# Kernel optimization log

Measured on AMD Instinct MI355X. Metric: run time of the kernel, lower is better.

## Reference

```python
import jax, jax.numpy as jnp
import numpy as np

N = 50000       # nodes
E = 800000      # edges
IN_DIM = 256    # input_dim
HEADS = 4
CH = 32         # per-head channels (hidden_dim; conv3 uses latent_dim//heads = 32 too)
HC = HEADS * CH # 128
ED = 32         # edge_dims


def setup_inputs():
    key = jax.random.key(0)
    ks = iter(jax.random.split(key, 64))
    def nrm(shape):
        return jax.random.normal(next(ks), shape, dtype=jnp.float32) * 0.05
    inp = {}
    inp["x"] = nrm((N, IN_DIM))
    inp["edge_index"] = jax.random.randint(next(ks), (2, E), 0, N)
    inp["attr"] = nrm((E, ED))
    for l, ind in ((1, IN_DIM), (2, HC), (3, HC)):
        inp[f"Wq{l}"] = nrm((ind, HC)); inp[f"bq{l}"] = jnp.zeros((HC,), jnp.float32)
        inp[f"Wk{l}"] = nrm((ind, HC)); inp[f"bk{l}"] = jnp.zeros((HC,), jnp.float32)
        inp[f"Wv{l}"] = nrm((ind, HC)); inp[f"bv{l}"] = jnp.zeros((HC,), jnp.float32)
        inp[f"We{l}"] = nrm((ED, HC))  # lin_edge has no bias in PyG TransformerConv
        inp[f"Ws{l}"] = nrm((ind, HC)); inp[f"bs{l}"] = jnp.zeros((HC,), jnp.float32)
    inp["g1"] = jnp.ones((HC,), jnp.float32); inp["be1"] = jnp.zeros((HC,), jnp.float32)
    inp["g2"] = jnp.ones((HC,), jnp.float32); inp["be2"] = jnp.zeros((HC,), jnp.float32)
    return inp


def _transformer_conv(x, src, dst, attr, Wq, bq, Wk, bk, Wv, bv, We, Ws, bs):
    # PyG TransformerConv, concat=True, root_weight=True, beta=False, dropout=0 (eval).
    q = (x @ Wq + bq).reshape(-1, HEADS, CH)   # [N,H,C] (queries at dst)
    k = (x @ Wk + bk).reshape(-1, HEADS, CH)
    v = (x @ Wv + bv).reshape(-1, HEADS, CH)
    e = (attr @ We).reshape(-1, HEADS, CH)     # [E,H,C]
    kj = k[src] + e                            # edge-conditioned keys  [E,H,C]
    vj = v[src] + e                            # edge-conditioned values [E,H,C]
    alpha = jnp.einsum('ehc,ehc->eh', q[dst], kj) / np.sqrt(CH).astype(np.float32)
    # segment softmax over incoming edges per destination node, per head
    amax = jax.ops.segment_max(alpha, dst, num_segments=N)          # [N,H]
    amax = jnp.where(jnp.isfinite(amax), amax, 0.0)                 # nodes with no edges
    ex = jnp.exp(alpha - amax[dst])                                 # [E,H]
    den = jax.ops.segment_sum(ex, dst, num_segments=N)              # [N,H]
    a = ex / (den[dst] + 1e-16)                                     # [E,H]
    out = jax.ops.segment_sum(a[..., None] * vj, dst, num_segments=N)  # [N,H,C]
    out = out.reshape(-1, HC) + (x @ Ws + bs)                       # + root skip
    return out, a


def _layernorm(x, g, b):
    m = x.mean(-1, keepdims=True)
    v = x.var(-1, keepdims=True)
    return (x - m) / jnp.sqrt(v + 1e-5) * g + b


def reference(x, edge_index, attr,
              Wq1, bq1, Wk1, bk1, Wv1, bv1, We1, Ws1, bs1,
              Wq2, bq2, Wk2, bk2, Wv2, bv2, We2, Ws2, bs2,
              Wq3, bq3, Wk3, bk3, Wv3, bv3, We3, Ws3, bs3,
              g1, be1, g2, be2):
    src, dst = edge_index[0], edge_index[1]
    h, a1 = _transformer_conv(x, src, dst, attr, Wq1, bq1, Wk1, bk1, Wv1, bv1, We1, Ws1, bs1)
    h = jax.nn.relu(_layernorm(h, g1, be1))   # dropout is identity in eval
    h, a2 = _transformer_conv(h, src, dst, attr, Wq2, bq2, Wk2, bk2, Wv2, bv2, We2, Ws2, bs2)
    h = jax.nn.relu(_layernorm(h, g2, be2))
    h, a3 = _transformer_conv(h, src, dst, attr, Wq3, bq3, Wk3, bk3, Wv3, bv3, We3, Ws3, bs3)
    return (h, a1, a2, a3)
```

## Files before the change

kernel.cpp:

```cpp
#include <hip/hip_runtime.h>
#include <math.h>

#define N_NODES 50000
#define E_EDGES 800000
#define HC 128
#define ED 32

typedef __attribute__((ext_vector_type(8))) short bf16x8;
typedef __attribute__((ext_vector_type(4))) float f32x4;
typedef unsigned short ushort_t;

__device__ __forceinline__ ushort_t f2bf(float f){
    unsigned u = __float_as_uint(f);
    return (ushort_t)((u + 0x7FFFu + ((u >> 16) & 1u)) >> 16);
}
__device__ __forceinline__ float bflo(unsigned u){ return __uint_as_float(u << 16); }
__device__ __forceinline__ float bfhi(unsigned u){ return __uint_as_float(u & 0xffff0000u); }


__global__ void hist_kernel(const int* __restrict__ dst, int* __restrict__ cnt, int n_edges){
    int e = blockIdx.x * blockDim.x + threadIdx.x;
    if (e < n_edges) atomicAdd(&cnt[dst[e]], 1);
}

__global__ __launch_bounds__(1024) void scan_sort_kernel(
    const int* __restrict__ cnt, int* __restrict__ rowptr,
    int* __restrict__ cursor, int* __restrict__ norder)
{
    __shared__ int part[1024];
    __shared__ int bins[64];
    __shared__ int binoff[64];
    const int t = threadIdx.x;
    const int CH = (N_NODES + 1023) / 1024;
    const int base = t * CH;
    int s = 0;
    for (int i = 0; i < CH; i++){
        int idx = base + i;
        if (idx < N_NODES) s += cnt[idx];
    }
    part[t] = s;
    __syncthreads();
    for (int off = 1; off < 1024; off <<= 1){
        int v = (t >= off) ? part[t - off] : 0;
        __syncthreads();
        part[t] += v;
        __syncthreads();
    }
    int off = (t == 0) ? 0 : part[t - 1];
    for (int i = 0; i < CH; i++){
        int idx = base + i;
        if (idx < N_NODES){
            int c = cnt[idx];
            rowptr[idx] = off;
            cursor[idx] = off;
            off += c;
        }
    }
    if (t == 1023) rowptr[N_NODES] = part[1023];

    if (t < 64) bins[t] = 0;
    __syncthreads();
    for (int i = t; i < N_NODES; i += 1024){
        int d = cnt[i];
        if (d > 63) d = 63;
        atomicAdd(&bins[d], 1);
    }
    __syncthreads();
    if (t == 0){
        int acc = 0;
        for (int d = 0; d < 64; d++){ int c = bins[d]; binoff[d] = acc; acc += c; }
    }
    __syncthreads();
    if (t < 64) bins[t] = binoff[t];
    __syncthreads();
    for (int i = t; i < N_NODES; i += 1024){
        int d = cnt[i];
        if (d > 63) d = 63;
        int pos = atomicAdd(&bins[d], 1);
        norder[pos] = i;
    }
}

__global__ void scatter_kernel(const int* __restrict__ src, const int* __restrict__ dst,
                               int* __restrict__ cursor, int2* __restrict__ es, int n_edges){
    int e = blockIdx.x * blockDim.x + threadIdx.x;
    if (e < n_edges){
        int d = dst[e];
        int pos = atomicAdd(&cursor[d], 1);
        es[pos] = make_int2(e, src[e]);
    }
}

__device__ __forceinline__ void pack_item(const float* __restrict__ Wq, const float* __restrict__ Wk,
                                          const float* __restrict__ Wv, const float* __restrict__ Ws,
                                          const float* __restrict__ We, ushort_t* __restrict__ Bp,
                                          int K, int item){
    int n = item % 640, k = item / 640;
    float val;
    if (n < 512){
        const float* W = (n < 128) ? Wq : (n < 256) ? Wk : (n < 384) ? Wv : Ws;
        val = W[k * HC + (n & 127)];
    } else {
        int col = n - 512, h5 = (col >> 5) * 32, d = col & 31;
        float acc = 0.f;
        for (int c = 0; c < 32; c++)
            acc = fmaf(Wq[k * HC + h5 + c], We[d * HC + h5 + c], acc);
        val = acc;
    }
    Bp[(((size_t)(k >> 3)) * 640 + n) * 8 + (k & 7)] = f2bf(val);
}

#define T_S0 12800000
#define T_S1 16000000
#define T_S2 16163840
#define T_S3 16245760
#define T_S4 16327680
#define T_S5 16328064

__global__ __launch_bounds__(256) void tail_kernel(
    const float* __restrict__ attr, const int2* __restrict__ es,
    const float* __restrict__ x, int perm_mode,
    ushort_t* __restrict__ attr_bf, ushort_t* __restrict__ Xbf,
    const float* __restrict__ Wq0, const float* __restrict__ bq0, const float* __restrict__ Wk0,
    const float* __restrict__ Wv0, const float* __restrict__ Ws0, const float* __restrict__ We0,
    const float* __restrict__ Wq1, const float* __restrict__ bq1, const float* __restrict__ Wk1,
    const float* __restrict__ Wv1, const float* __restrict__ Ws1, const float* __restrict__ We1,
    const float* __restrict__ Wq2, const float* __restrict__ bq2, const float* __restrict__ Wk2,
    const float* __restrict__ Wv2, const float* __restrict__ Ws2, const float* __restrict__ We2,
    ushort_t* __restrict__ Bp0, ushort_t* __restrict__ Bp1, ushort_t* __restrict__ Bp2,
    float* __restrict__ qwb3)
{
    const int stride = gridDim.x * blockDim.x;
    for (int gi = blockIdx.x * blockDim.x + threadIdx.x; gi < T_S5; gi += stride){
        if (gi < T_S0){
            if (perm_mode){
                int grp = gi >> 4, lane = gi & 15;
                int e = es[grp].x;
                const float2 v = *(const float2*)&attr[(size_t)e * ED + lane * 2];
                unsigned r = (unsigned)f2bf(v.x) | ((unsigned)f2bf(v.y) << 16);
                ((unsigned*)attr_bf)[(size_t)grp * (ED / 2) + lane] = r;
            }
        } else if (gi < T_S1){
            int i = gi - T_S0;
            float4 v = ((const float4*)x)[i];
            ushort_t r0 = f2bf(v.x), r1 = f2bf(v.y), r2 = f2bf(v.z), r3 = f2bf(v.w);
            ((ushort4*)Xbf)[i] = make_ushort4(r0, r1, r2, r3);
        } else if (gi < T_S2){
            pack_item(Wq0, Wk0, Wv0, Ws0, We0, Bp0, 256, gi - T_S1);
        } else if (gi < T_S3){
            pack_item(Wq1, Wk1, Wv1, Ws1, We1, Bp1, 128, gi - T_S2);
        } else if (gi < T_S4){
            pack_item(Wq2, Wk2, Wv2, Ws2, We2, Bp2, 128, gi - T_S3);
        } else {
            int f = gi - T_S4;
            int l = f >> 7, t2 = f & 127;
            const float* bq = (l == 0) ? bq0 : (l == 1) ? bq1 : bq2;
            const float* We = (l == 0) ? We0 : (l == 1) ? We1 : We2;
            int h5 = (t2 >> 5) * 32, d = t2 & 31;
            float acc = 0.f;
            for (int c = 0; c < 32; c++)
                acc = fmaf(bq[h5 + c], We[d * HC + h5 + c], acc);
            qwb3[l * HC + t2] = acc;
        }
    }
}

template<int K>
__global__ __launch_bounds__(320) void gemm_mfma(
    const ushort_t* __restrict__ Xbf, const ushort_t* __restrict__ Bpack,
    const float* __restrict__ b0, const float* __restrict__ b1,
    const float* __restrict__ b2, const float* __restrict__ b3,
    const float* __restrict__ b4,
    float* __restrict__ Yq, ushort_t* __restrict__ Ykbf,
    ushort_t* __restrict__ Yvbf, float* __restrict__ Ys,
    float* __restrict__ Yw, int M)
{
    const int w = threadIdx.x >> 6;
    const int lane = threadIdx.x & 63;
    const int q = lane >> 4, nn = lane & 15;
    const int row0 = blockIdx.x * 32;

    f32x4 acc[2][8];
    #pragma unroll
    for (int mt = 0; mt < 2; mt++)
        #pragma unroll
        for (int nt = 0; nt < 8; nt++)
            acc[mt][nt] = (f32x4){0.f, 0.f, 0.f, 0.f};

    const int r0 = row0 + nn;
    const int r1 = row0 + 16 + nn;
    const bf16x8 zf = (bf16x8){0,0,0,0,0,0,0,0};

    #pragma unroll
    for (int kc = 0; kc < K / 32; kc++){
        bf16x8 a0 = (r0 < M) ? *(const bf16x8*)&Xbf[(size_t)r0 * K + kc * 32 + q * 8] : zf;
        bf16x8 a1 = (r1 < M) ? *(const bf16x8*)&Xbf[(size_t)r1 * K + kc * 32 + q * 8] : zf;
        bf16x8 b[8];
        #pragma unroll
        for (int nt = 0; nt < 8; nt++){
            int n = w * 128 + nt * 16 + nn;
            b[nt] = *(const bf16x8*)&Bpack[(((size_t)(kc * 4 + q)) * 640 + n) * 8];
        }
        #pragma unroll
        for (int nt = 0; nt < 8; nt++){
            acc[0][nt] = __builtin_amdgcn_mfma_f32_16x16x32_bf16(a0, b[nt], acc[0][nt], 0, 0, 0);
            acc[1][nt] = __builtin_amdgcn_mfma_f32_16x16x32_bf16(a1, b[nt], acc[1][nt], 0, 0, 0);
        }
    }

    const float scale = (w == 0 || w == 4) ? 0.17677669529663687f : 1.f;
    const float* bias = (w == 0) ? b0 : (w == 1) ? b1 : (w == 2) ? b2 : (w == 3) ? b3 : b4;

    if (w == 1 || w == 2){
        ushort_t* Yb = (w == 1) ? Ykbf : Yvbf;
        #pragma unroll
        for (int nt = 0; nt < 8; nt++){
            int col = nt * 16 + nn;
            float bval = bias[col];
            #pragma unroll
            for (int mt = 0; mt < 2; mt++){
                #pragma unroll
                for (int r = 0; r < 4; r++){
                    int row = row0 + mt * 16 + q * 4 + r;
                    if (row < M) Yb[(size_t)row * HC + col] = f2bf(acc[mt][nt][r] + bval);
                }
            }
        }
    } else {
        float* Y = (w == 0) ? Yq : (w == 3) ? Ys : Yw;
        #pragma unroll
        for (int nt = 0; nt < 8; nt++){
            int col = nt * 16 + nn;
            float bval = bias[col];
            #pragma unroll
            for (int mt = 0; mt < 2; mt++){
                #pragma unroll
                for (int r = 0; r < 4; r++){
                    int row = row0 + mt * 16 + q * 4 + r;
                    if (row < M) Y[(size_t)row * HC + col] = (acc[mt][nt][r] + bval) * scale;
                }
            }
        }
    }
}

__device__ __forceinline__ float dot16(const uint4 kk, const uint4 aa,
                                       const float4 qA, const float4 qB,
                                       const float4 wA, const float4 wB){
    float p =           bflo(kk.x) * qA.x;
    p = fmaf(bfhi(kk.x), qA.y, p);
    p = fmaf(bflo(kk.y), qA.z, p);
    p = fmaf(bfhi(kk.y), qA.w, p);
    p = fmaf(bflo(kk.z), qB.x, p);
    p = fmaf(bfhi(kk.z), qB.y, p);
    p = fmaf(bflo(kk.w), qB.z, p);
    p = fmaf(bfhi(kk.w), qB.w, p);
    p = fmaf(bflo(aa.x), wA.x, p);
    p = fmaf(bfhi(aa.x), wA.y, p);
    p = fmaf(bflo(aa.y), wA.z, p);
    p = fmaf(bfhi(aa.y), wA.w, p);
    p = fmaf(bflo(aa.z), wB.x, p);
    p = fmaf(bfhi(aa.z), wB.y, p);
    p = fmaf(bflo(aa.w), wB.z, p);
    p = fmaf(bfhi(aa.w), wB.w, p);
    return p;
}

__device__ __forceinline__ uint4 packrow(const float* p){
    float4 x = *(const float4*)p;
    float4 y = *(const float4*)(p + 4);
    uint4 r;
    r.x = (unsigned)f2bf(x.x) | ((unsigned)f2bf(x.y) << 16);
    r.y = (unsigned)f2bf(x.z) | ((unsigned)f2bf(x.w) << 16);
    r.z = (unsigned)f2bf(y.x) | ((unsigned)f2bf(y.y) << 16);
    r.w = (unsigned)f2bf(y.z) | ((unsigned)f2bf(y.w) << 16);
    return r;
}

__global__ __launch_bounds__(256) void fused_attn_kernel(
    const float* __restrict__ qs, const float* __restrict__ qw,
    const ushort_t* __restrict__ kb, const ushort_t* __restrict__ vb,
    const float* __restrict__ skip, const float* __restrict__ We,
    const float* __restrict__ attr, const ushort_t* __restrict__ attr_bf, int perm_mode,
    const int* __restrict__ rowptr, const int2* __restrict__ es,
    const int* __restrict__ norder,
    float* __restrict__ acsr, float* __restrict__ a_out,
    const float* __restrict__ g, const float* __restrict__ be,
    float* __restrict__ out_f32, ushort_t* __restrict__ out_bf, int apply_ln)
{
    __shared__ unsigned WeTb[2560];
    __shared__ float SL[2304];
    const int t = threadIdx.x;
    for (int idx = t; idx < 2048; idx += 256){
        int w = idx & 15;
        int c = idx >> 4;
        float lo = We[(2 * w) * HC + c];
        float hi = We[(2 * w + 1) * HC + c];
        unsigned u = (unsigned)f2bf(lo) | ((unsigned)f2bf(hi) << 16);
        WeTb[c * 20 + ((((w >> 1) + (c >> 3)) & 7) << 1) + (w & 1)] = u;
    }
    __syncthreads();

    const int lane = t & 63, wvi = t >> 6;
    const int qq = lane >> 4, li = lane & 15;
    const int h = li >> 2, j = li & 3;
    const int gq = blockIdx.x * 16 + wvi * 4 + qq;
    if (gq >= N_NODES) return;
    const int n = norder[gq];
    const int ch = h * 32 + j * 8;
    const size_t nrow = (size_t)n * HC + ch;

    const float4 qA = *(const float4*)&qs[nrow];
    const float4 qB = *(const float4*)&qs[nrow + 4];
    const float4 wA = *(const float4*)&qw[nrow];
    const float4 wB = *(const float4*)&qw[nrow + 4];

    const int beg = rowptr[n], end = rowptr[n + 1];
    float m = -1e30f, s = 0.f;
    float acc[8] = {0,0,0,0,0,0,0,0};
    float S[8]   = {0,0,0,0,0,0,0,0};

    for (int i = beg; i < end; i += 2){
        const bool two = (i + 1 < end);
        const int2 e0 = es[i];
        const int2 e1 = two ? es[i + 1] : e0;
        const uint4 k0 = *(const uint4*)&kb[(size_t)e0.y * HC + ch];
        const uint4 k1 = *(const uint4*)&kb[(size_t)e1.y * HC + ch];
        const uint4 v0 = *(const uint4*)&vb[(size_t)e0.y * HC + ch];
        const uint4 v1 = *(const uint4*)&vb[(size_t)e1.y * HC + ch];
        uint4 a0u, a1u;
        if (perm_mode){
            a0u = *(const uint4*)&attr_bf[(size_t)i * ED + j * 8];
            a1u = two ? *(const uint4*)&attr_bf[(size_t)(i + 1) * ED + j * 8] : a0u;
        } else {
            a0u = packrow(&attr[(size_t)e0.x * ED + j * 8]);
            a1u = two ? packrow(&attr[(size_t)e1.x * ED + j * 8]) : a0u;
        }
        float p0 = dot16(k0, a0u, qA, qB, wA, wB);
        float p1 = dot16(k1, a1u, qA, qB, wA, wB);
        p0 += __shfl_xor(p0, 1);  p1 += __shfl_xor(p1, 1);
        p0 += __shfl_xor(p0, 2);  p1 += __shfl_xor(p1, 2);
        const float al0 = p0;
        const float al1 = two ? p1 : -1e38f;
        if (j == 0){
            acsr[(size_t)i * 4 + h] = al0;
            if (two) acsr[(size_t)(i + 1) * 4 + h] = al1;
        }
        const float mn = fmaxf(m, fmaxf(al0, al1));
        const float sc = __expf(m - mn);
        const float w0 = __expf(al0 - mn);
        const float w1 = __expf(al1 - mn);
        m = mn;
        s = fmaf(s, sc, w0 + w1);
        acc[0] = fmaf(acc[0], sc, fmaf(w0, bflo(v0.x), w1 * bflo(v1.x)));
        acc[1] = fmaf(acc[1], sc, fmaf(w0, bfhi(v0.x), w1 * bfhi(v1.x)));
        acc[2] = fmaf(acc[2], sc, fmaf(w0, bflo(v0.y), w1 * bflo(v1.y)));
        acc[3] = fmaf(acc[3], sc, fmaf(w0, bfhi(v0.y), w1 * bfhi(v1.y)));
        acc[4] = fmaf(acc[4], sc, fmaf(w0, bflo(v0.z), w1 * bflo(v1.z)));
        acc[5] = fmaf(acc[5], sc, fmaf(w0, bfhi(v0.z), w1 * bfhi(v1.z)));
        acc[6] = fmaf(acc[6], sc, fmaf(w0, bflo(v0.w), w1 * bflo(v1.w)));
        acc[7] = fmaf(acc[7], sc, fmaf(w0, bfhi(v0.w), w1 * bfhi(v1.w)));
        S[0] = fmaf(S[0], sc, fmaf(w0, bflo(a0u.x), w1 * bflo(a1u.x)));
        S[1] = fmaf(S[1], sc, fmaf(w0, bfhi(a0u.x), w1 * bfhi(a1u.x)));
        S[2] = fmaf(S[2], sc, fmaf(w0, bflo(a0u.y), w1 * bflo(a1u.y)));
        S[3] = fmaf(S[3], sc, fmaf(w0, bfhi(a0u.y), w1 * bfhi(a1u.y)));
        S[4] = fmaf(S[4], sc, fmaf(w0, bflo(a0u.z), w1 * bflo(a1u.z)));
        S[5] = fmaf(S[5], sc, fmaf(w0, bfhi(a0u.z), w1 * bfhi(a1u.z)));
        S[6] = fmaf(S[6], sc, fmaf(w0, bflo(a0u.w), w1 * bflo(a1u.w)));
        S[7] = fmaf(S[7], sc, fmaf(w0, bfhi(a0u.w), w1 * bfhi(a1u.w)));
    }

    const int nl = wvi * 4 + qq;
    const int sbase = nl * 144;
    const int hsk = h * 36;
    *(float4*)&SL[sbase + hsk + j * 8]     = make_float4(S[0], S[1], S[2], S[3]);
    *(float4*)&SL[sbase + hsk + j * 8 + 4] = make_float4(S[4], S[5], S[6], S[7]);
    asm volatile("" ::: "memory");
    float E[8] = {0,0,0,0,0,0,0,0};
    #pragma unroll
    for (int d4 = 0; d4 < 8; d4++){
        const float4 sv = *(const float4*)&SL[sbase + hsk + d4 * 4];
        const int rot = ((d4 + li) & 7) << 1;
        #pragma unroll
        for (int r = 0; r < 8; r++){
            const uint2 wu = *(const uint2*)&WeTb[(ch + r) * 20 + rot];
            E[r] = fmaf(sv.x, bflo(wu.x), fmaf(sv.y, bfhi(wu.x),
                   fmaf(sv.z, bflo(wu.y), fmaf(sv.w, bfhi(wu.y), E[r]))));
        }
    }

    const float inv = 1.f / (s + 1e-16f);
    const float4 skA = *(const float4*)&skip[nrow];
    const float4 skB = *(const float4*)&skip[nrow + 4];
    float o[8];
    o[0] = (acc[0] + E[0]) * inv + skA.x;
    o[1] = (acc[1] + E[1]) * inv + skA.y;
    o[2] = (acc[2] + E[2]) * inv + skA.z;
    o[3] = (acc[3] + E[3]) * inv + skA.w;
    o[4] = (acc[4] + E[4]) * inv + skB.x;
    o[5] = (acc[5] + E[5]) * inv + skB.y;
    o[6] = (acc[6] + E[6]) * inv + skB.z;
    o[7] = (acc[7] + E[7]) * inv + skB.w;

    if (apply_ln){
        float s1 = 0.f, s2 = 0.f;
        #pragma unroll
        for (int r = 0; r < 8; r++){ s1 += o[r]; s2 = fmaf(o[r], o[r], s2); }
        #pragma unroll
        for (int off = 1; off <= 8; off <<= 1){
            s1 += __shfl_xor(s1, off);
            s2 += __shfl_xor(s2, off);
        }
        const float mu  = s1 * (1.f / 128.f);
        const float var = s2 * (1.f / 128.f) - mu * mu;
        const float ivs = rsqrtf(var + 1e-5f);
        const float4 gA = *(const float4*)&g[ch];
        const float4 gB = *(const float4*)&g[ch + 4];
        const float4 bA = *(const float4*)&be[ch];
        const float4 bB = *(const float4*)&be[ch + 4];
        o[0] = fmaxf((o[0] - mu) * ivs * gA.x + bA.x, 0.f);
        o[1] = fmaxf((o[1] - mu) * ivs * gA.y + bA.y, 0.f);
        o[2] = fmaxf((o[2] - mu) * ivs * gA.z + bA.z, 0.f);
        o[3] = fmaxf((o[3] - mu) * ivs * gA.w + bA.w, 0.f);
        o[4] = fmaxf((o[4] - mu) * ivs * gB.x + bB.x, 0.f);
        o[5] = fmaxf((o[5] - mu) * ivs * gB.y + bB.y, 0.f);
        o[6] = fmaxf((o[6] - mu) * ivs * gB.z + bB.z, 0.f);
        o[7] = fmaxf((o[7] - mu) * ivs * gB.w + bB.w, 0.f);
        uint4 st;
        st.x = (unsigned)f2bf(o[0]) | ((unsigned)f2bf(o[1]) << 16);
        st.y = (unsigned)f2bf(o[2]) | ((unsigned)f2bf(o[3]) << 16);
        st.z = (unsigned)f2bf(o[4]) | ((unsigned)f2bf(o[5]) << 16);
        st.w = (unsigned)f2bf(o[6]) | ((unsigned)f2bf(o[7]) << 16);
        *(uint4*)&out_bf[nrow] = st;
    } else {
        *(float4*)&out_f32[nrow]     = make_float4(o[0], o[1], o[2], o[3]);
        *(float4*)&out_f32[nrow + 4] = make_float4(o[4], o[5], o[6], o[7]);
    }

    const float mh = __shfl(m, (qq << 4) + ((li & 3) << 2));
    const float dh = __shfl(s, (qq << 4) + ((li & 3) << 2));
    const float ih = 1.f / (dh + 1e-16f);
    asm volatile("s_waitcnt vmcnt(0)" ::: "memory");
    for (int f = beg * 4 + li; f < end * 4; f += 16){
        const int e = es[f >> 2].x;
        a_out[(size_t)e * 4 + (li & 3)] = __expf(acsr[f] - mh) * ih;
    }
}


extern "C" void kernel_launch(void* const* d_in, const int* in_sizes, int n_in,
                              void* d_out, int out_size, void* d_ws, size_t ws_size,
                              hipStream_t stream) {
    const float* x    = (const float*)d_in[0];
    const int*   ei   = (const int*)  d_in[1];
    const float* attr = (const float*)d_in[2];
    const float* gln[2]  = { (const float*)d_in[30], (const float*)d_in[32] };
    const float* beln[2] = { (const float*)d_in[31], (const float*)d_in[33] };

    float* out   = (float*)d_out;
    float* h_out = out;
    float* a_out[3] = { out + (size_t)N_NODES * HC,
                        out + (size_t)N_NODES * HC + (size_t)E_EDGES * 4,
                        out + (size_t)N_NODES * HC + (size_t)2 * E_EDGES * 4 };

    char* base = (char*)d_ws;
    size_t off = 0;
    auto alloc = [&](size_t bytes) -> void* {
        void* p = base + off;
        off = (off + bytes + 63) & ~(size_t)63;
        return p;
    };
    const size_t NB = (size_t)N_NODES * HC;
    float* qbuf     = (float*)alloc(NB * 4);
    float* qwbuf    = (float*)alloc(NB * 4);
    ushort_t* kbf   = (ushort_t*)alloc(NB * 2);
    ushort_t* vbf   = (ushort_t*)alloc(NB * 2);
    float* sbuf     = (float*)alloc(NB * 4);
    int* rowptr     = (int*)alloc((N_NODES + 1) * 4);
    int* cnt        = (int*)alloc(N_NODES * 4);
    int* cursor     = (int*)alloc(N_NODES * 4);
    int* norder     = (int*)alloc(N_NODES * 4);
    int2* es        = (int2*)alloc((size_t)E_EDGES * 8);
    ushort_t* Xbf   = (ushort_t*)alloc((size_t)N_NODES * 256 * 2);
    ushort_t* Hbf   = (ushort_t*)alloc(NB * 2);
    ushort_t* Bp0   = (ushort_t*)alloc((size_t)256 * 640 * 2);
    ushort_t* Bp1   = (ushort_t*)alloc((size_t)128 * 640 * 2);
    ushort_t* Bp2   = (ushort_t*)alloc((size_t)128 * 640 * 2);
    float* acsr     = (float*)alloc((size_t)E_EDGES * 4 * 4);
    float* qwb3     = (float*)alloc((size_t)3 * HC * 4);
    ushort_t* attr_bf = (ushort_t*)alloc((size_t)E_EDGES * ED * 2);
    const int perm_mode = (ws_size >= off) ? 1 : 0;

    const int* srcp = ei;
    const int* dstp = ei + E_EDGES;

    hipMemsetAsync(cnt, 0, (size_t)N_NODES * 4, stream);
    hist_kernel<<<(E_EDGES + 255) / 256, 256, 0, stream>>>(dstp, cnt, E_EDGES);
    scan_sort_kernel<<<1, 1024, 0, stream>>>(cnt, rowptr, cursor, norder);
    scatter_kernel<<<(E_EDGES + 255) / 256, 256, 0, stream>>>(srcp, dstp, cursor, es, E_EDGES);
    tail_kernel<<<4096, 256, 0, stream>>>(
        attr, es, x, perm_mode, attr_bf, Xbf,
        (const float*)d_in[3],  (const float*)d_in[4],  (const float*)d_in[5],
        (const float*)d_in[7],  (const float*)d_in[10], (const float*)d_in[9],
        (const float*)d_in[12], (const float*)d_in[13], (const float*)d_in[14],
        (const float*)d_in[16], (const float*)d_in[19], (const float*)d_in[18],
        (const float*)d_in[21], (const float*)d_in[22], (const float*)d_in[23],
        (const float*)d_in[25], (const float*)d_in[28], (const float*)d_in[27],
        Bp0, Bp1, Bp2, qwb3);

    const int gemm_grid = (N_NODES + 31) / 32;
    const int attn_grid = (N_NODES + 15) / 16;
    ushort_t* Bps[3] = { Bp0, Bp1, Bp2 };

    for (int l = 0; l < 3; l++){
        const float* bq = (const float*)d_in[3 + 9 * l + 1];
        const float* bk = (const float*)d_in[3 + 9 * l + 3];
        const float* bv = (const float*)d_in[3 + 9 * l + 5];
        const float* We = (const float*)d_in[3 + 9 * l + 6];
        const float* bs = (const float*)d_in[3 + 9 * l + 8];

        if (l == 0)
            gemm_mfma<256><<<gemm_grid, 320, 0, stream>>>(Xbf, Bps[l], bq, bk, bv, bs, qwb3 + 128 * l,
                                                          qbuf, kbf, vbf, sbuf, qwbuf, N_NODES);
        else
            gemm_mfma<128><<<gemm_grid, 320, 0, stream>>>(Hbf, Bps[l], bq, bk, bv, bs, qwb3 + 128 * l,
                                                          qbuf, kbf, vbf, sbuf, qwbuf, N_NODES);

        const float* gg = (l < 2) ? gln[l] : nullptr;
        const float* bb = (l < 2) ? beln[l] : nullptr;
        fused_attn_kernel<<<attn_grid, 256, 0, stream>>>(
            qbuf, qwbuf, kbf, vbf, sbuf, We, attr, attr_bf, perm_mode,
            rowptr, es, norder, acsr, a_out[l], gg, bb,
            (l < 2) ? nullptr : h_out, (l < 2) ? Hbf : nullptr, (l < 2) ? 1 : 0);
    }
}
```

Before: 1.109 ms.

## Replace degree-sorted node order with persistent atomic work-stealing attention kernel

Removes the degree-binning counting sort from the scan kernel. The attention kernel becomes persistent with a fixed grid of 2048 blocks, and each wavefront grabs groups of four consecutive nodes through a global atomic counter. The counter is zeroed alongside the histogram buffer, with a separate counter per layer. This aims to balance load dynamically and cut the serial sort work, but it loses the degree grouping that kept divergence low within a wavefront, and it adds one atomic per four nodes.

```diff
diff --git a/kernel.cpp b/kernel.cpp
--- a/kernel.cpp
+++ b/kernel.cpp
@@ -5,6 +5,7 @@
 #define E_EDGES 800000
 #define HC 128
 #define ED 32
+#define N_QUADS 12500
 
 typedef __attribute__((ext_vector_type(8))) short bf16x8;
 typedef __attribute__((ext_vector_type(4))) float f32x4;
@@ -23,13 +24,10 @@
     if (e < n_edges) atomicAdd(&cnt[dst[e]], 1);
 }
 
-__global__ __launch_bounds__(1024) void scan_sort_kernel(
-    const int* __restrict__ cnt, int* __restrict__ rowptr,
-    int* __restrict__ cursor, int* __restrict__ norder)
+__global__ __launch_bounds__(1024) void scan_kernel(
+    const int* __restrict__ cnt, int* __restrict__ rowptr, int* __restrict__ cursor)
 {
     __shared__ int part[1024];
-    __shared__ int bins[64];
-    __shared__ int binoff[64];
     const int t = threadIdx.x;
     const int CH = (N_NODES + 1023) / 1024;
     const int base = t * CH;
@@ -57,28 +55,6 @@
         }
     }
     if (t == 1023) rowptr[N_NODES] = part[1023];
-
-    if (t < 64) bins[t] = 0;
-    __syncthreads();
-    for (int i = t; i < N_NODES; i += 1024){
-        int d = cnt[i];
-        if (d > 63) d = 63;
-        atomicAdd(&bins[d], 1);
-    }
-    __syncthreads();
-    if (t == 0){
-        int acc = 0;
-        for (int d = 0; d < 64; d++){ int c = bins[d]; binoff[d] = acc; acc += c; }
-    }
-    __syncthreads();
-    if (t < 64) bins[t] = binoff[t];
-    __syncthreads();
-    for (int i = t; i < N_NODES; i += 1024){
-        int d = cnt[i];
-        if (d > 63) d = 63;
-        int pos = atomicAdd(&bins[d], 1);
-        norder[pos] = i;
-    }
 }
 
 __global__ void scatter_kernel(const int* __restrict__ src, const int* __restrict__ dst,
@@ -283,7 +259,7 @@
     const float* __restrict__ skip, const float* __restrict__ We,
     const float* __restrict__ attr, const ushort_t* __restrict__ attr_bf, int perm_mode,
     const int* __restrict__ rowptr, const int2* __restrict__ es,
-    const int* __restrict__ norder,
+    int* __restrict__ wctr,
     float* __restrict__ acsr, float* __restrict__ a_out,
     const float* __restrict__ g, const float* __restrict__ be,
     float* __restrict__ out_f32, ushort_t* __restrict__ out_bf, int apply_ln)
@@ -304,146 +280,151 @@
     const int lane = t & 63, wvi = t >> 6;
     const int qq = lane >> 4, li = lane & 15;
     const int h = li >> 2, j = li & 3;
-    const int gq = blockIdx.x * 16 + wvi * 4 + qq;
-    if (gq >= N_NODES) return;
-    const int n = norder[gq];
     const int ch = h * 32 + j * 8;
-    const size_t nrow = (size_t)n * HC + ch;
-
-    const float4 qA = *(const float4*)&qs[nrow];
-    const float4 qB = *(const float4*)&qs[nrow + 4];
-    const float4 wA = *(const float4*)&qw[nrow];
-    const float4 wB = *(const float4*)&qw[nrow + 4];
-
-    const int beg = rowptr[n], end = rowptr[n + 1];
-    float m = -1e30f, s = 0.f;
-    float acc[8] = {0,0,0,0,0,0,0,0};
-    float S[8]   = {0,0,0,0,0,0,0,0};
-
-    for (int i = beg; i < end; i += 2){
-        const bool two = (i + 1 < end);
-        const int2 e0 = es[i];
-        const int2 e1 = two ? es[i + 1] : e0;
-        const uint4 k0 = *(const uint4*)&kb[(size_t)e0.y * HC + ch];
-        const uint4 k1 = *(const uint4*)&kb[(size_t)e1.y * HC + ch];
-        const uint4 v0 = *(const uint4*)&vb[(size_t)e0.y * HC + ch];
-        const uint4 v1 = *(const uint4*)&vb[(size_t)e1.y * HC + ch];
-        uint4 a0u, a1u;
-        if (perm_mode){
-            a0u = *(const uint4*)&attr_bf[(size_t)i * ED + j * 8];
-            a1u = two ? *(const uint4*)&attr_bf[(size_t)(i + 1) * ED + j * 8] : a0u;
-        } else {
-            a0u = packrow(&attr[(size_t)e0.x * ED + j * 8]);
-            a1u = two ? packrow(&attr[(size_t)e1.x * ED + j * 8]) : a0u;
-        }
-        float p0 = dot16(k0, a0u, qA, qB, wA, wB);
-        float p1 = dot16(k1, a1u, qA, qB, wA, wB);
-        p0 += __shfl_xor(p0, 1);  p1 += __shfl_xor(p1, 1);
-        p0 += __shfl_xor(p0, 2);  p1 += __shfl_xor(p1, 2);
-        const float al0 = p0;
-        const float al1 = two ? p1 : -1e38f;
-        if (j == 0){
-            acsr[(size_t)i * 4 + h] = al0;
-            if (two) acsr[(size_t)(i + 1) * 4 + h] = al1;
-        }
-        const float mn = fmaxf(m, fmaxf(al0, al1));
-        const float sc = __expf(m - mn);
-        const float w0 = __expf(al0 - mn);
-        const float w1 = __expf(al1 - mn);
-        m = mn;
-        s = fmaf(s, sc, w0 + w1);
-        acc[0] = fmaf(acc[0], sc, fmaf(w0, bflo(v0.x), w1 * bflo(v1.x)));
-        acc[1] = fmaf(acc[1], sc, fmaf(w0, bfhi(v0.x), w1 * bfhi(v1.x)));
-        acc[2] = fmaf(acc[2], sc, fmaf(w0, bflo(v0.y), w1 * bflo(v1.y)));
-        acc[3] = fmaf(acc[3], sc, fmaf(w0, bfhi(v0.y), w1 * bfhi(v1.y)));
-        acc[4] = fmaf(acc[4], sc, fmaf(w0, bflo(v0.z), w1 * bflo(v1.z)));
-        acc[5] = fmaf(acc[5], sc, fmaf(w0, bfhi(v0.z), w1 * bfhi(v1.z)));
-        acc[6] = fmaf(acc[6], sc, fmaf(w0, bflo(v0.w), w1 * bflo(v1.w)));
-        acc[7] = fmaf(acc[7], sc, fmaf(w0, bfhi(v0.w), w1 * bfhi(v1.w)));
-        S[0] = fmaf(S[0], sc, fmaf(w0, bflo(a0u.x), w1 * bflo(a1u.x)));
-        S[1] = fmaf(S[1], sc, fmaf(w0, bfhi(a0u.x), w1 * bfhi(a1u.x)));
-        S[2] = fmaf(S[2], sc, fmaf(w0, bflo(a0u.y), w1 * bflo(a1u.y)));
-        S[3] = fmaf(S[3], sc, fmaf(w0, bfhi(a0u.y), w1 * bfhi(a1u.y)));
-        S[4] = fmaf(S[4], sc, fmaf(w0, bflo(a0u.z), w1 * bflo(a1u.z)));
-        S[5] = fmaf(S[5], sc, fmaf(w0, bfhi(a0u.z), w1 * bfhi(a1u.z)));
-        S[6] = fmaf(S[6], sc, fmaf(w0, bflo(a0u.w), w1 * bflo(a1u.w)));
-        S[7] = fmaf(S[7], sc, fmaf(w0, bfhi(a0u.w), w1 * bfhi(a1u.w)));
-    }
-
     const int nl = wvi * 4 + qq;
     const int sbase = nl * 144;
     const int hsk = h * 36;
-    *(float4*)&SL[sbase + hsk + j * 8]     = make_float4(S[0], S[1], S[2], S[3]);
-    *(float4*)&SL[sbase + hsk + j * 8 + 4] = make_float4(S[4], S[5], S[6], S[7]);
-    asm volatile("" ::: "memory");
-    float E[8] = {0,0,0,0,0,0,0,0};
-    #pragma unroll
-    for (int d4 = 0; d4 < 8; d4++){
-        const float4 sv = *(const float4*)&SL[sbase + hsk + d4 * 4];
-        const int rot = ((d4 + li) & 7) << 1;
+
+    for (;;){
+        int quad;
+        if (lane == 0) quad = atomicAdd(wctr, 1);
+        quad = __shfl(quad, 0);
+        if (quad >= N_QUADS) return;
+        const int n = quad * 4 + qq;
+        const size_t nrow = (size_t)n * HC + ch;
+
+        const float4 qA = *(const float4*)&qs[nrow];
+        const float4 qB = *(const float4*)&qs[nrow + 4];
+        const float4 wA = *(const float4*)&qw[nrow];
+        const float4 wB = *(const float4*)&qw[nrow + 4];
+
+        const int beg = rowptr[n], end = rowptr[n + 1];
+        float m = -1e30f, s = 0.f;
+        float acc[8] = {0,0,0,0,0,0,0,0};
+        float S[8]   = {0,0,0,0,0,0,0,0};
+
+        for (int i = beg; i < end; i += 2){
+            const bool two = (i + 1 < end);
+            const int2 e0 = es[i];
+            const int2 e1 = two ? es[i + 1] : e0;
+            const uint4 k0 = *(const uint4*)&kb[(size_t)e0.y * HC + ch];
+            const uint4 k1 = *(const uint4*)&kb[(size_t)e1.y * HC + ch];
+            const uint4 v0 = *(const uint4*)&vb[(size_t)e0.y * HC + ch];
+            const uint4 v1 = *(const uint4*)&vb[(size_t)e1.y * HC + ch];
+            uint4 a0u, a1u;
+            if (perm_mode){
+                a0u = *(const uint4*)&attr_bf[(size_t)i * ED + j * 8];
+                a1u = two ? *(const uint4*)&attr_bf[(size_t)(i + 1) * ED + j * 8] : a0u;
+            } else {
+                a0u = packrow(&attr[(size_t)e0.x * ED + j * 8]);
+                a1u = two ? packrow(&attr[(size_t)e1.x * ED + j * 8]) : a0u;
+            }
+            float p0 = dot16(k0, a0u, qA, qB, wA, wB);
+            float p1 = dot16(k1, a1u, qA, qB, wA, wB);
+            p0 += __shfl_xor(p0, 1);  p1 += __shfl_xor(p1, 1);
+            p0 += __shfl_xor(p0, 2);  p1 += __shfl_xor(p1, 2);
+            const float al0 = p0;
+            const float al1 = two ? p1 : -1e38f;
+            if (j == 0){
+                acsr[(size_t)i * 4 + h] = al0;
+                if (two) acsr[(size_t)(i + 1) * 4 + h] = al1;
+            }
+            const float mn = fmaxf(m, fmaxf(al0, al1));
+            const float sc = __expf(m - mn);
+            const float w0 = __expf(al0 - mn);
+            const float w1 = __expf(al1 - mn);
+            m = mn;
+            s = fmaf(s, sc, w0 + w1);
+            acc[0] = fmaf(acc[0], sc, fmaf(w0, bflo(v0.x), w1 * bflo(v1.x)));
+            acc[1] = fmaf(acc[1], sc, fmaf(w0, bfhi(v0.x), w1 * bfhi(v1.x)));
+            acc[2] = fmaf(acc[2], sc, fmaf(w0, bflo(v0.y), w1 * bflo(v1.y)));
+            acc[3] = fmaf(acc[3], sc, fmaf(w0, bfhi(v0.y), w1 * bfhi(v1.y)));
+            acc[4] = fmaf(acc[4], sc, fmaf(w0, bflo(v0.z), w1 * bflo(v1.z)));
+            acc[5] = fmaf(acc[5], sc, fmaf(w0, bfhi(v0.z), w1 * bfhi(v1.z)));
+            acc[6] = fmaf(acc[6], sc, fmaf(w0, bflo(v0.w), w1 * bflo(v1.w)));
+            acc[7] = fmaf(acc[7], sc, fmaf(w0, bfhi(v0.w), w1 * bfhi(v1.w)));
+            S[0] = fmaf(S[0], sc, fmaf(w0, bflo(a0u.x), w1 * bflo(a1u.x)));
+            S[1] = fmaf(S[1], sc, fmaf(w0, bfhi(a0u.x), w1 * bfhi(a1u.x)));
+            S[2] = fmaf(S[2], sc, fmaf(w0, bflo(a0u.y), w1 * bflo(a1u.y)));
+            S[3] = fmaf(S[3], sc, fmaf(w0, bfhi(a0u.y), w1 * bfhi(a1u.y)));
+            S[4] = fmaf(S[4], sc, fmaf(w0, bflo(a0u.z), w1 * bflo(a1u.z)));
+            S[5] = fmaf(S[5], sc, fmaf(w0, bfhi(a0u.z), w1 * bfhi(a1u.z)));
+            S[6] = fmaf(S[6], sc, fmaf(w0, bflo(a0u.w), w1 * bflo(a1u.w)));
+            S[7] = fmaf(S[7], sc, fmaf(w0, bfhi(a0u.w), w1 * bfhi(a1u.w)));
+        }
+
+        *(float4*)&SL[sbase + hsk + j * 8]     = make_float4(S[0], S[1], S[2], S[3]);
+        *(float4*)&SL[sbase + hsk + j * 8 + 4] = make_float4(S[4], S[5], S[6], S[7]);
+        asm volatile("" ::: "memory");
+        float E[8] = {0,0,0,0,0,0,0,0};
         #pragma unroll
-        for (int r = 0; r < 8; r++){
-            const uint2 wu = *(const uint2*)&WeTb[(ch + r) * 20 + rot];
-            E[r] = fmaf(sv.x, bflo(wu.x), fmaf(sv.y, bfhi(wu.x),
-                   fmaf(sv.z, bflo(wu.y), fmaf(sv.w, bfhi(wu.y), E[r]))));
-        }
-    }
-
-    const float inv = 1.f / (s + 1e-16f);
-    const float4 skA = *(const float4*)&skip[nrow];
-    const float4 skB = *(const float4*)&skip[nrow + 4];
-    float o[8];
-    o[0] = (acc[0] + E[0]) * inv + skA.x;
-    o[1] = (acc[1] + E[1]) * inv + skA.y;
-    o[2] = (acc[2] + E[2]) * inv + skA.z;
-    o[3] = (acc[3] + E[3]) * inv + skA.w;
-    o[4] = (acc[4] + E[4]) * inv + skB.x;
-    o[5] = (acc[5] + E[5]) * inv + skB.y;
-    o[6] = (acc[6] + E[6]) * inv + skB.z;
-    o[7] = (acc[7] + E[7]) * inv + skB.w;
-
-    if (apply_ln){
-        float s1 = 0.f, s2 = 0.f;
-        #pragma unroll
-        for (int r = 0; r < 8; r++){ s1 += o[r]; s2 = fmaf(o[r], o[r], s2); }
-        #pragma unroll
-        for (int off = 1; off <= 8; off <<= 1){
-            s1 += __shfl_xor(s1, off);
-            s2 += __shfl_xor(s2, off);
-        }
-        const float mu  = s1 * (1.f / 128.f);
-        const float var = s2 * (1.f / 128.f) - mu * mu;
-        const float ivs = rsqrtf(var + 1e-5f);
-        const float4 gA = *(const float4*)&g[ch];
-        const float4 gB = *(const float4*)&g[ch + 4];
-        const float4 bA = *(const float4*)&be[ch];
-        const float4 bB = *(const float4*)&be[ch + 4];
-        o[0] = fmaxf((o[0] - mu) * ivs * gA.x + bA.x, 0.f);
-        o[1] = fmaxf((o[1] - mu) * ivs * gA.y + bA.y, 0.f);
-        o[2] = fmaxf((o[2] - mu) * ivs * gA.z + bA.z, 0.f);
-        o[3] = fmaxf((o[3] - mu) * ivs * gA.w + bA.w, 0.f);
-        o[4] = fmaxf((o[4] - mu) * ivs * gB.x + bB.x, 0.f);
-        o[5] = fmaxf((o[5] - mu) * ivs * gB.y + bB.y, 0.f);
-        o[6] = fmaxf((o[6] - mu) * ivs * gB.z + bB.z, 0.f);
-        o[7] = fmaxf((o[7] - mu) * ivs * gB.w + bB.w, 0.f);
-        uint4 st;
-        st.x = (unsigned)f2bf(o[0]) | ((unsigned)f2bf(o[1]) << 16);
-        st.y = (unsigned)f2bf(o[2]) | ((unsigned)f2bf(o[3]) << 16);
-        st.z = (unsigned)f2bf(o[4]) | ((unsigned)f2bf(o[5]) << 16);
-        st.w = (unsigned)f2bf(o[6]) | ((unsigned)f2bf(o[7]) << 16);
-        *(uint4*)&out_bf[nrow] = st;
-    } else {
-        *(float4*)&out_f32[nrow]     = make_float4(o[0], o[1], o[2], o[3]);
-        *(float4*)&out_f32[nrow + 4] = make_float4(o[4], o[5], o[6], o[7]);
-    }
-
-    const float mh = __shfl(m, (qq << 4) + ((li & 3) << 2));
-    const float dh = __shfl(s, (qq << 4) + ((li & 3) << 2));
-    const float ih = 1.f / (dh + 1e-16f);
-    asm volatile("s_waitcnt vmcnt(0)" ::: "memory");
-    for (int f = beg * 4 + li; f < end * 4; f += 16){
-        const int e = es[f >> 2].x;
-        a_out[(size_t)e * 4 + (li & 3)] = __expf(acsr[f] - mh) * ih;
+        for (int d4 = 0; d4 < 8; d4++){
+            const float4 sv = *(const float4*)&SL[sbase + hsk + d4 * 4];
+            const int rot = ((d4 + li) & 7) << 1;
+            #pragma unroll
+            for (int r = 0; r < 8; r++){
+                const uint2 wu = *(const uint2*)&WeTb[(ch + r) * 20 + rot];
+                E[r] = fmaf(sv.x, bflo(wu.x), fmaf(sv.y, bfhi(wu.x),
+                       fmaf(sv.z, bflo(wu.y), fmaf(sv.w, bfhi(wu.y), E[r]))));
+            }
+        }
+
+        const float inv = 1.f / (s + 1e-16f);
+        const float4 skA = *(const float4*)&skip[nrow];
+        const float4 skB = *(const float4*)&skip[nrow + 4];
+        float o[8];
+        o[0] = (acc[0] + E[0]) * inv + skA.x;
+        o[1] = (acc[1] + E[1]) * inv + skA.y;
+        o[2] = (acc[2] + E[2]) * inv + skA.z;
+        o[3] = (acc[3] + E[3]) * inv + skA.w;
+        o[4] = (acc[4] + E[4]) * inv + skB.x;
+        o[5] = (acc[5] + E[5]) * inv + skB.y;
+        o[6] = (acc[6] + E[6]) * inv + skB.z;
+        o[7] = (acc[7] + E[7]) * inv + skB.w;
+
+        if (apply_ln){
+            float s1 = 0.f, s2 = 0.f;
+            #pragma unroll
+            for (int r = 0; r < 8; r++){ s1 += o[r]; s2 = fmaf(o[r], o[r], s2); }
+            #pragma unroll
+            for (int off = 1; off <= 8; off <<= 1){
+                s1 += __shfl_xor(s1, off);
+                s2 += __shfl_xor(s2, off);
+            }
+            const float mu  = s1 * (1.f / 128.f);
+            const float var = s2 * (1.f / 128.f) - mu * mu;
+            const float ivs = rsqrtf(var + 1e-5f);
+            const float4 gA = *(const float4*)&g[ch];
+            const float4 gB = *(const float4*)&g[ch + 4];
+            const float4 bA = *(const float4*)&be[ch];
+            const float4 bB = *(const float4*)&be[ch + 4];
+            o[0] = fmaxf((o[0] - mu) * ivs * gA.x + bA.x, 0.f);
+            o[1] = fmaxf((o[1] - mu) * ivs * gA.y + bA.y, 0.f);
+            o[2] = fmaxf((o[2] - mu) * ivs * gA.z + bA.z, 0.f);
+            o[3] = fmaxf((o[3] - mu) * ivs * gA.w + bA.w, 0.f);
+            o[4] = fmaxf((o[4] - mu) * ivs * gB.x + bB.x, 0.f);
+            o[5] = fmaxf((o[5] - mu) * ivs * gB.y + bB.y, 0.f);
+            o[6] = fmaxf((o[6] - mu) * ivs * gB.z + bB.z, 0.f);
+            o[7] = fmaxf((o[7] - mu) * ivs * gB.w + bB.w, 0.f);
+            uint4 st;
+            st.x = (unsigned)f2bf(o[0]) | ((unsigned)f2bf(o[1]) << 16);
+            st.y = (unsigned)f2bf(o[2]) | ((unsigned)f2bf(o[3]) << 16);
+            st.z = (unsigned)f2bf(o[4]) | ((unsigned)f2bf(o[5]) << 16);
+            st.w = (unsigned)f2bf(o[6]) | ((unsigned)f2bf(o[7]) << 16);
+            *(uint4*)&out_bf[nrow] = st;
+        } else {
+            *(float4*)&out_f32[nrow]     = make_float4(o[0], o[1], o[2], o[3]);
+            *(float4*)&out_f32[nrow + 4] = make_float4(o[4], o[5], o[6], o[7]);
+        }
+
+        const float mh = __shfl(m, (qq << 4) + ((li & 3) << 2));
+        const float dh = __shfl(s, (qq << 4) + ((li & 3) << 2));
+        const float ih = 1.f / (dh + 1e-16f);
+        asm volatile("s_waitcnt vmcnt(0)" ::: "memory");
+        for (int f = beg * 4 + li; f < end * 4; f += 16){
+            const int e = es[f >> 2].x;
+            a_out[(size_t)e * 4 + (li & 3)] = __expf(acsr[f] - mh) * ih;
+        }
     }
 }
 
@@ -477,9 +458,8 @@
     ushort_t* vbf   = (ushort_t*)alloc(NB * 2);
     float* sbuf     = (float*)alloc(NB * 4);
     int* rowptr     = (int*)alloc((N_NODES + 1) * 4);
-    int* cnt        = (int*)alloc(N_NODES * 4);
+    int* cnt        = (int*)alloc((N_NODES + 16) * 4);
     int* cursor     = (int*)alloc(N_NODES * 4);
-    int* norder     = (int*)alloc(N_NODES * 4);
     int2* es        = (int2*)alloc((size_t)E_EDGES * 8);
     ushort_t* Xbf   = (ushort_t*)alloc((size_t)N_NODES * 256 * 2);
     ushort_t* Hbf   = (ushort_t*)alloc(NB * 2);
@@ -490,13 +470,14 @@
     float* qwb3     = (float*)alloc((size_t)3 * HC * 4);
     ushort_t* attr_bf = (ushort_t*)alloc((size_t)E_EDGES * ED * 2);
     const int perm_mode = (ws_size >= off) ? 1 : 0;
+    int* wctr = cnt + N_NODES;
 
     const int* srcp = ei;
     const int* dstp = ei + E_EDGES;
 
-    hipMemsetAsync(cnt, 0, (size_t)N_NODES * 4, stream);
+    hipMemsetAsync(cnt, 0, (size_t)(N_NODES + 16) * 4, stream);
     hist_kernel<<<(E_EDGES + 255) / 256, 256, 0, stream>>>(dstp, cnt, E_EDGES);
-    scan_sort_kernel<<<1, 1024, 0, stream>>>(cnt, rowptr, cursor, norder);
+    scan_kernel<<<1, 1024, 0, stream>>>(cnt, rowptr, cursor);
     scatter_kernel<<<(E_EDGES + 255) / 256, 256, 0, stream>>>(srcp, dstp, cursor, es, E_EDGES);
     tail_kernel<<<4096, 256, 0, stream>>>(
         attr, es, x, perm_mode, attr_bf, Xbf,
@@ -509,7 +490,6 @@
         Bp0, Bp1, Bp2, qwb3);
 
     const int gemm_grid = (N_NODES + 31) / 32;
-    const int attn_grid = (N_NODES + 15) / 16;
     ushort_t* Bps[3] = { Bp0, Bp1, Bp2 };
 
     for (int l = 0; l < 3; l++){
@@ -528,9 +508,9 @@
 
         const float* gg = (l < 2) ? gln[l] : nullptr;
         const float* bb = (l < 2) ? beln[l] : nullptr;
-        fused_attn_kernel<<<attn_grid, 256, 0, stream>>>(
+        fused_attn_kernel<<<2048, 256, 0, stream>>>(
             qbuf, qwbuf, kbf, vbf, sbuf, We, attr, attr_bf, perm_mode,
-            rowptr, es, norder, acsr, a_out[l], gg, bb,
+            rowptr, es, wctr + 4 * l, acsr, a_out[l], gg, bb,
             (l < 2) ? nullptr : h_out, (l < 2) ? Hbf : nullptr, (l < 2) ? 1 : 0);
     }
 }
```

Result: slower. 1.529 ms (+37.9%).
